# Kernel optimization log

Hardware: AMD Instinct MI355X
Metric: run time of the kernel (lower is better)

Reference implementation:

```python
import jax, jax.numpy as jnp
import numpy as np
import math

NLAT, NLON, LMAX, MMAX = 128, 256, 50, 50
M = NLAT * NLON  # = 2*NLAT^2 grid points, matches torch meshgrid(arange(nlat), arange(-nlat,nlat))

def _grid_np():
    gx, gy = np.meshgrid(np.arange(NLAT), np.arange(-NLAT, NLAT), indexing='ij')
    g = np.stack([gx.ravel(), gy.ravel()], -1).astype(np.float32)
    return g / NLAT * np.pi  # (M, 2)

def _cc_weights(n):
    # Clenshaw-Curtis quadrature nodes theta_j = pi*j/(n-1) and weights on [-1,1]
    N = n - 1
    theta = np.pi * np.arange(n) / N
    k = np.arange(1, N // 2 + 1)
    b = np.where(2 * k == N, 1.0, 2.0)
    S = (b / (4.0 * k ** 2 - 1.0) * np.cos(2.0 * np.outer(theta, k))).sum(-1)
    w = (2.0 / N) * (1.0 - S)
    w[0] *= 0.5
    w[-1] *= 0.5
    return theta, w

def _legendre(lmax, mmax, theta):
    # orthonormal (4pi-normalized) associated Legendre P_l^m(cos theta), Condon-Shortley phase
    x, s = np.cos(theta), np.sin(theta)
    P = np.zeros((mmax, lmax, theta.shape[0]))
    P[0, 0] = math.sqrt(1.0 / (4.0 * math.pi))
    pmm = P[0, 0].copy()
    for m in range(1, mmax):
        pmm = -math.sqrt((2 * m + 1) / (2.0 * m)) * s * pmm
        P[m, m] = pmm
    for m in range(mmax):
        if m + 1 < lmax:
            P[m, m + 1] = math.sqrt(2 * m + 3.0) * x * P[m, m]
        for l in range(m + 2, lmax):
            a = math.sqrt((4.0 * l * l - 1.0) / (l * l - m * m))
            bb = math.sqrt(((l - 1.0) ** 2 - m * m) / (4.0 * (l - 1.0) ** 2 - 1.0))
            P[m, l] = a * (x * P[m, l - 1] - bb * P[m, l - 2])
    return P

_theta_q, _wq = _cc_weights(NLAT)
_SHT_W = jnp.asarray((_legendre(LMAX, MMAX, _theta_q) * _wq).astype(np.float32))  # (mmax, lmax, nlat)
_GRID = jnp.asarray(_grid_np())  # (M, 2)

def setup_inputs() -> dict:
    key = jax.random.key(0)
    target = jax.random.normal(key, (2, 2048, 3), dtype=jnp.float32)
    return {"target": target}

def reference(target):
    B, N, _ = target.shape
    # to_spherical: rho=(B,N) features, sph=(phi, theta)-pi shift on theta -> (B,N,2)
    rho = jnp.linalg.norm(target, axis=-1)
    phi = jnp.arctan2(target[..., 1], target[..., 0])
    theta = jnp.arccos(target[..., 2] / rho)
    sph = jnp.stack([phi, theta - jnp.pi], axis=-1)  # (B, N, 2)
    # squared distances grid(M,2) vs sph(B,N,2) -> (B,M,N) via gram trick (no (B,M,N,2) temp)
    s2 = jnp.sum(sph * sph, -1)                 # (B, N)
    g2 = jnp.sum(_GRID * _GRID, -1)             # (M,)
    cross = jnp.einsum('md,bnd->bmn', _GRID, sph)
    D2 = jax.lax.stop_gradient(s2[:, None, :] + g2[None, :, None] - 2.0 * cross)
    _, idx = jax.lax.top_k(-D2, 3)              # (B, M, 3), 3-NN targets per grid point, ascending dist
    bidx = jnp.arange(B)[:, None, None]
    tmp = sph[bidx, idx]                        # (B, M, 3, 2)
    dist = jnp.sqrt(jnp.sum((tmp - _GRID[None, :, None, :]) ** 2, -1))  # (B, M, 3)
    w = dist / jnp.sum(dist, -1, keepdims=True)
    # three_interpolate: weighted combine of rho at 3 NNs -> (B, M)
    interp = jnp.sum(rho[bidx, idx] * w, -1)
    f = interp.reshape(B, NLAT, NLON)
    # RealSHT (equiangular grid): forward-normalized rfft over lon, then Legendre contraction over lat
    F = (2.0 * jnp.pi) * jnp.fft.rfft(f, axis=-1) / NLON  # (B, nlat, nlon//2+1) complex
    coeff_re = jnp.einsum('bkm,mlk->blm', jnp.real(F[..., :MMAX]), _SHT_W)  # (B, lmax, mmax)
    return coeff_re
```

## Files before the change

kernel.cpp:

```cpp
#include <hip/hip_runtime.h>
#include <math.h>
#include <stdint.h>

#define NLAT 128
#define NLON 256
#define LMAX 50
#define MMAX 50
#define MGRID (NLAT*NLON)
#define BATCH 2
#define NPTS 2048
#define NBKT 64
#define NSRT 2056
#define PI_F 3.14159265358979323846f

typedef float v2f __attribute__((ext_vector_type(2)));

__device__ __forceinline__ uint32_t umin32(uint32_t a, uint32_t b) { return a < b ? a : b; }
__device__ __forceinline__ uint32_t umax32(uint32_t a, uint32_t b) { return a > b ? a : b; }

#define WS_F    0
#define WS_SXY  65536
#define WS_SR   (WS_SXY + BATCH*NSRT*2)
#define WS_BST  (WS_SR + BATCH*NSRT)
#define WS_WG   78080
#define WS_CT   (WS_WG + MMAX*LMAX*NLAT)

__global__ __launch_bounds__(512)
void k_prep(const float* __restrict__ target, float* __restrict__ ws) {
    __shared__ __attribute__((aligned(16))) float2 s_all[NSRT];
    __shared__ float    s_rall[NSRT];
    __shared__ int      cnt[NBKT], start[NBKT + 1], cur[NBKT];
    __shared__ float    s_a[LMAX], s_bb[LMAX], s_w[NLAT];
    __shared__ float    s_cm;
    int blk = blockIdx.x;
    int tid = threadIdx.x;

    if (blk < BATCH) {
        const float* tg = target + blk * NPTS * 3;
        if (tid < NBKT) cnt[tid] = 0;
        __syncthreads();
        float ph[4], py[4], rh[4]; int bk[4];
        #pragma unroll
        for (int c = 0; c < 4; ++c) {
            int p = tid + c * 512;
            float x = tg[p*3], y = tg[p*3+1], z = tg[p*3+2];
            float r = sqrtf(fmaf(x, x, fmaf(y, y, z*z)));
            float cc = fminf(1.f, fmaxf(-1.f, z / r));
            float pyv = acosf(cc) - PI_F;
            ph[c] = atan2f(y, x); py[c] = pyv; rh[c] = r;
            int bb = (int)floorf((pyv + PI_F) * ((float)NBKT / PI_F));
            bk[c] = min(NBKT-1, max(0, bb));
            atomicAdd(&cnt[bk[c]], 1);
        }
        __syncthreads();
        if (tid < 64) {
            int v = cnt[tid];
            int cv = v;
            #pragma unroll
            for (int sh = 1; sh < 64; sh <<= 1) {
                int t = __shfl_up(v, sh);
                if (tid >= sh) v += t;
            }
            start[tid + 1] = v;
            cur[tid] = v - cv;
            if (tid == 0) start[0] = 0;
        }
        __syncthreads();
        #pragma unroll
        for (int c = 0; c < 4; ++c) {
            int pos = atomicAdd(&cur[bk[c]], 1);
            s_all[pos]  = make_float2(ph[c], py[c]);
            s_rall[pos] = rh[c];
        }
        if (tid < 8) {
            s_all[NPTS + tid] = make_float2(1e15f, 1e15f);
            s_rall[NPTS + tid] = 0.f;
        }
        __syncthreads();
        float2* gxy = (float2*)(ws + WS_SXY) + blk * NSRT;
        float*  gr  = ws + WS_SR + blk * NSRT;
        int*    bst = (int*)(ws + WS_BST) + blk * (NBKT + 1);
        for (int t = tid; t < NSRT; t += 512) { gxy[t] = s_all[t]; gr[t] = s_rall[t]; }
        if (tid <= NBKT) bst[tid] = start[tid];
    } else {
        int m = blk - BATCH;
        if (tid < 64) {
            int i = tid;
            float v = (i >= 1 && i <= m)
                      ? 0.5f * __log2f((2.f*i + 1.f) / (2.f*i)) : 0.f;
            #pragma unroll
            for (int sh = 1; sh < 64; sh <<= 1) v += __shfl_xor(v, sh);
            if (i == 0) s_cm = ((m & 1) ? -1.f : 1.f) * exp2f(v);
        } else if (tid < 128) {
            int l = tid - 64;
            if (l < LMAX) {
                float fl = (float)l, fm2 = (float)(m*m);
                s_a[l]  = sqrtf((4.f*fl*fl - 1.f) / fmaxf(fl*fl - fm2, 0.25f));
                float flm1 = fl - 1.f;
                s_bb[l] = sqrtf(fmaxf(flm1*flm1 - fm2, 0.f) /
                                fmaxf(4.f*flm1*flm1 - 1.f, 0.25f));
            }
        } else if (tid < 256) {
            int k = tid - 128;
            float theta = (PI_F * (float)k) / 127.0f;
            float S = 0.0f;
            for (int kk = 1; kk <= 63; ++kk)
                S += 2.0f / (4.0f*kk*kk - 1.0f) * __cosf(2.0f * theta * (float)kk);
            float w = (2.0f/127.0f) * (1.0f - S);
            if (k == 0 || k == NLAT-1) w *= 0.5f;
            s_w[k] = w;
        } else {
            int j = tid - 256;
            ws[WS_CT + m*256 + j] =
                __cosf((float)((m * j) & 255) * (2.0f*PI_F/256.0f));
        }
        __syncthreads();
        if (tid < NLAT) {
            int k = tid;
            float* Wm = ws + WS_WG + m * (LMAX * NLAT);
            float theta = (PI_F * (float)k) / 127.0f;
            float x = __cosf(theta), sn = __sinf(theta);
            float w = s_w[k];
            float pmm;
            if (m == 0) pmm = 0.28209479177f;
            else {
                float mag = exp2f((float)m * __log2f(fabsf(sn)));
                float sg  = (sn < 0.f && (m & 1)) ? -1.f : 1.f;
                pmm = 0.28209479177f * s_cm * mag * sg;
            }
            for (int l = 0; l < m; ++l) Wm[l*NLAT + k] = 0.0f;
            float Plm2 = pmm;
            Wm[m*NLAT + k] = Plm2 * w;
            if (m + 1 < LMAX) {
                float Plm1 = sqrtf(2.0f*m + 3.0f) * x * pmm;
                Wm[(m+1)*NLAT + k] = Plm1 * w;
                for (int l = m + 2; l < LMAX; ++l) {
                    float P = s_a[l] * fmaf(-s_bb[l], Plm2, x * Plm1);
                    Wm[l*NLAT + k] = P * w;
                    Plm2 = Plm1; Plm1 = P;
                }
            }
        }
    }
}

__global__ __launch_bounds__(512, 2)
void k_nn(const float* __restrict__ ws_c, float* __restrict__ f) {
    __shared__ __attribute__((aligned(16))) float2 s_all[NSRT];
    __shared__ float    s_rall[NSRT];
    __shared__ uint32_t s_keys[8*64*3];
    __shared__ int      s_start[NBKT + 1];
    __shared__ int      s_win[2];
    int b = blockIdx.x >> 8;
    int j = blockIdx.x & 255;
    int tid = threadIdx.x;

    if (tid <= NBKT)
        s_start[tid] = ((const int*)(ws_c + WS_BST))[b*(NBKT+1) + tid];
    __syncthreads();

    float gy = (float)(j - 128) * (PI_F / 128.0f);
    int c0 = (int)floorf((gy + PI_F) * ((float)NBKT / PI_F));
    c0 = min(NBKT-1, max(0, c0));
    if (tid < 64) {
        int t = tid;
        int lo_t = max(0, c0 - 5 - t), hi_t = min(NBKT-1, c0 + 5 + t);
        int cw_t = s_start[hi_t+1] - s_start[lo_t];
        unsigned long long ok =
            __ballot(cw_t >= 192 || (lo_t == 0 && hi_t == NBKT-1));
        int t0 = __ffsll((unsigned long long)ok) - 1;
        if (tid == 0) {
            s_win[0] = max(0, c0 - 5 - t0);
            s_win[1] = min(NBKT-1, c0 + 5 + t0);
        }
    }
    __syncthreads();

    int lo = s_win[0], hi = s_win[1];
    int off0 = s_start[lo];
    int cw   = s_start[hi+1] - off0;
    int n    = cw + 8;
    const float2* gxy = (const float2*)(ws_c + WS_SXY) + b * NSRT + off0;
    const float*  gr  = ws_c + WS_SR + b * NSRT + off0;
    for (int t = tid; t < n; t += 512) { s_all[t] = gxy[t]; s_rall[t] = gr[t]; }
    __syncthreads();

    int q = ((cw + 3) / 4 + 1) & ~1;
    int lane = tid & 63;
    int wv   = tid >> 6;
    int part = wv & 3;
    int lat  = lane + ((wv >> 2) << 6);
    float gx = (float)lat * (PI_F / 128.0f);
    v2f gx2 = {gx, gx}, gy2 = {gy, gy};
    uint32_t k0 = ~0u, k1 = ~0u, k2 = ~0u;
    uint32_t nb = (uint32_t)(part * q);
    const float4* p4 = (const float4*)(s_all + part * q);
    int iters = q >> 1;
    #pragma unroll 4
    for (int i = 0; i < iters; ++i) {
        float4 Q = p4[i];
        v2f px = {Q.x, Q.z}, pyy = {Q.y, Q.w};
        v2f dp = gx2 - px, dt = gy2 - pyy;
        v2f d = dp * dp;
        d = dt * dt + d;
        uint32_t key0 = (__float_as_uint(d.x) & 0xFFFFF800u) | (nb + 2u*i);
        uint32_t key1 = (__float_as_uint(d.y) & 0xFFFFF800u) | (nb + 2u*i + 1u);
        uint32_t t1;
        t1 = umin32(umax32(key0, k0), k1);
        k2 = umin32(umax32(key0, k1), k2);
        k0 = umin32(key0, k0); k1 = t1;
        t1 = umin32(umax32(key1, k0), k1);
        k2 = umin32(umax32(key1, k1), k2);
        k0 = umin32(key1, k0); k1 = t1;
    }
    s_keys[(wv*64 + lane)*3 + 0] = k0;
    s_keys[(wv*64 + lane)*3 + 1] = k1;
    s_keys[(wv*64 + lane)*3 + 2] = k2;
    __syncthreads();

    if (tid < 128) {
        int lane2 = tid & 63;
        int half  = tid >> 6;
        uint32_t m0 = ~0u, m1 = ~0u, m2 = ~0u;
        #pragma unroll
        for (int w = half*4; w < half*4 + 4; ++w) {
            #pragma unroll
            for (int s = 0; s < 3; ++s) {
                uint32_t key = s_keys[(w*64 + lane2)*3 + s];
                uint32_t t1 = umin32(umax32(key, m0), m1);
                m2 = umin32(umax32(key, m1), m2);
                m0 = umin32(key, m0); m1 = t1;
            }
        }
        int i0 = (int)(m0 & 2047);
        int i1 = (int)(m1 & 2047);
        int i2 = (int)(m2 & 2047);
        int lat2 = lane2 + (half << 6);
        float gxs = (float)lat2 * (PI_F / 128.0f);
        float2 p0 = s_all[i0], p1 = s_all[i1], p2 = s_all[i2];
        float e, r0, r1, r2;
        e = gxs - p0.x; r0 = e*e; e = gy - p0.y; r0 = sqrtf(fmaf(e, e, r0));
        e = gxs - p1.x; r1 = e*e; e = gy - p1.y; r1 = sqrtf(fmaf(e, e, r1));
        e = gxs - p2.x; r2 = e*e; e = gy - p2.y; r2 = sqrtf(fmaf(e, e, r2));
        float sum = r0 + r1 + r2;
        float interp = (s_rall[i0]*r0 + s_rall[i1]*r1 + s_rall[i2]*r2) / sum;
        f[b * MGRID + lat2 * NLON + j] = interp;
    }
}

__global__ __launch_bounds__(512)
void k_fft(const float* __restrict__ f, const float* __restrict__ ws_c,
           float* __restrict__ out) {
    __shared__ float red[NLAT*5];
    __shared__ float sFre[NLAT];
    __shared__ float cred[256];
    __shared__ float ct_s[256];
    int b = blockIdx.x / MMAX;
    int m = blockIdx.x % MMAX;
    int tid = threadIdx.x;

    if (tid < 256) ct_s[tid] = ws_c[WS_CT + m*256 + tid];
    __syncthreads();

    {
        int k = tid >> 2, g = tid & 3;
        const float4* fb4 = (const float4*)(f + b * MGRID);
        float p = 0.0f;
        int j0 = g * 64;
        #pragma unroll
        for (int i = 0; i < 16; ++i) {
            float4 v = fb4[k * 64 + g * 16 + i];
            p = fmaf(v.x, ct_s[j0 + 4*i    ], p);
            p = fmaf(v.y, ct_s[j0 + 4*i + 1], p);
            p = fmaf(v.z, ct_s[j0 + 4*i + 2], p);
            p = fmaf(v.w, ct_s[j0 + 4*i + 3], p);
        }
        red[k * 5 + g] = p;
    }
    __syncthreads();

    if (tid < NLAT) {
        int k = tid;
        sFre[k] = (red[k*5] + red[k*5+1] + red[k*5+2] + red[k*5+3])
                  * (2.0f * PI_F / 256.0f);
    }
    __syncthreads();

    float acc = 0.0f;
    if (tid < 200) {
        int l = tid >> 2, kq = tid & 3;
        const float* Wm = ws_c + WS_WG + (m * LMAX + l) * NLAT;
        #pragma unroll 8
        for (int i = 0; i < 32; ++i)
            acc = fmaf(Wm[kq*32 + i], sFre[kq*32 + i], acc);
    }
    if (tid < 256) cred[tid] = acc;
    __syncthreads();
    if (tid < LMAX)
        out[(b*LMAX + tid)*MMAX + m] =
            cred[4*tid] + cred[4*tid+1] + cred[4*tid+2] + cred[4*tid+3];
}

extern "C" void kernel_launch(void* const* d_in, const int* in_sizes, int n_in,
                              void* d_out, int out_size, void* d_ws, size_t ws_size,
                              hipStream_t stream) {
    const float* target = (const float*)d_in[0];
    float* out = (float*)d_out;
    float* ws  = (float*)d_ws;
    float* f   = ws + WS_F;

    k_prep<<<BATCH + MMAX, 512, 0, stream>>>(target, ws);
    k_nn  <<<BATCH * NLON, 512, 0, stream>>>(ws, f);
    k_fft <<<BATCH * MMAX, 512, 0, stream>>>(f, ws, out);
}
```

Before: 77.39 us.

## Fuse prep, NN interpolation and SHT into one cooperative kernel with grid syncs

Merges the three kernels into a single cooperative launch of 256 blocks, separating the phases with grid-wide syncs instead of kernel boundaries. Each block now handles two longitude columns in the NN phase, where before it handled one across 512 blocks. This removes two launch gaps and the tail effects between them. In exchange it halves the block count in the NN phase, adds grid-sync overhead, and raises register and LDS pressure because one kernel now declares every phase's shared arrays.

```diff
diff --git a/kernel.cpp b/kernel.cpp
--- a/kernel.cpp
+++ b/kernel.cpp
@@ -1,6 +1,9 @@
 #include <hip/hip_runtime.h>
+#include <hip/hip_cooperative_groups.h>
 #include <math.h>
 #include <stdint.h>
+
+namespace cg = cooperative_groups;
 
 #define NLAT 128
 #define NLON 256
@@ -25,13 +28,21 @@
 #define WS_WG   78080
 #define WS_CT   (WS_WG + MMAX*LMAX*NLAT)
 
-__global__ __launch_bounds__(512)
-void k_prep(const float* __restrict__ target, float* __restrict__ ws) {
+__global__ __launch_bounds__(512, 2)
+void k_fused(const float* __restrict__ target, float* ws, float* out) {
     __shared__ __attribute__((aligned(16))) float2 s_all[NSRT];
     __shared__ float    s_rall[NSRT];
-    __shared__ int      cnt[NBKT], start[NBKT + 1], cur[NBKT];
+    __shared__ uint32_t s_keys[8*64*3];
+    __shared__ int      cnt[NBKT], s_start[NBKT + 1], cur[NBKT];
+    __shared__ int      s_win[2];
     __shared__ float    s_a[LMAX], s_bb[LMAX], s_w[NLAT];
     __shared__ float    s_cm;
+    __shared__ float    red[NLAT*5];
+    __shared__ float    sFre[NLAT];
+    __shared__ float    cred[256];
+    __shared__ float    ct_s[256];
+
+    cg::grid_group grid = cg::this_grid();
     int blk = blockIdx.x;
     int tid = threadIdx.x;
 
@@ -61,9 +72,9 @@
                 int t = __shfl_up(v, sh);
                 if (tid >= sh) v += t;
             }
-            start[tid + 1] = v;
+            s_start[tid + 1] = v;
             cur[tid] = v - cv;
-            if (tid == 0) start[0] = 0;
+            if (tid == 0) s_start[0] = 0;
         }
         __syncthreads();
         #pragma unroll
@@ -81,8 +92,8 @@
         float*  gr  = ws + WS_SR + blk * NSRT;
         int*    bst = (int*)(ws + WS_BST) + blk * (NBKT + 1);
         for (int t = tid; t < NSRT; t += 512) { gxy[t] = s_all[t]; gr[t] = s_rall[t]; }
-        if (tid <= NBKT) bst[tid] = start[tid];
-    } else {
+        if (tid <= NBKT) bst[tid] = s_start[tid];
+    } else if (blk < BATCH + MMAX) {
         int m = blk - BATCH;
         if (tid < 64) {
             int i = tid;
@@ -142,163 +153,157 @@
             }
         }
     }
-}
-
-__global__ __launch_bounds__(512, 2)
-void k_nn(const float* __restrict__ ws_c, float* __restrict__ f) {
-    __shared__ __attribute__((aligned(16))) float2 s_all[NSRT];
-    __shared__ float    s_rall[NSRT];
-    __shared__ uint32_t s_keys[8*64*3];
-    __shared__ int      s_start[NBKT + 1];
-    __shared__ int      s_win[2];
-    int b = blockIdx.x >> 8;
-    int j = blockIdx.x & 255;
-    int tid = threadIdx.x;
-
-    if (tid <= NBKT)
-        s_start[tid] = ((const int*)(ws_c + WS_BST))[b*(NBKT+1) + tid];
-    __syncthreads();
-
-    float gy = (float)(j - 128) * (PI_F / 128.0f);
-    int c0 = (int)floorf((gy + PI_F) * ((float)NBKT / PI_F));
-    c0 = min(NBKT-1, max(0, c0));
-    if (tid < 64) {
-        int t = tid;
-        int lo_t = max(0, c0 - 5 - t), hi_t = min(NBKT-1, c0 + 5 + t);
-        int cw_t = s_start[hi_t+1] - s_start[lo_t];
-        unsigned long long ok =
-            __ballot(cw_t >= 192 || (lo_t == 0 && hi_t == NBKT-1));
-        int t0 = __ffsll((unsigned long long)ok) - 1;
-        if (tid == 0) {
-            s_win[0] = max(0, c0 - 5 - t0);
-            s_win[1] = min(NBKT-1, c0 + 5 + t0);
+    __threadfence();
+    grid.sync();
+
+    {
+        int b  = blk >> 7;
+        int jj = blk & 127;
+        if (tid <= NBKT)
+            s_start[tid] = ((const int*)(ws + WS_BST))[b*(NBKT+1) + tid];
+        __syncthreads();
+
+        for (int cidx = 0; cidx < 2; ++cidx) {
+            int j = jj * 2 + cidx;
+            float gy = (float)(j - 128) * (PI_F / 128.0f);
+            int c0 = (int)floorf((gy + PI_F) * ((float)NBKT / PI_F));
+            c0 = min(NBKT-1, max(0, c0));
+            if (tid < 64) {
+                int t = tid;
+                int lo_t = max(0, c0 - 5 - t), hi_t = min(NBKT-1, c0 + 5 + t);
+                int cw_t = s_start[hi_t+1] - s_start[lo_t];
+                unsigned long long ok =
+                    __ballot(cw_t >= 192 || (lo_t == 0 && hi_t == NBKT-1));
+                int t0 = __ffsll((unsigned long long)ok) - 1;
+                if (tid == 0) {
+                    s_win[0] = max(0, c0 - 5 - t0);
+                    s_win[1] = min(NBKT-1, c0 + 5 + t0);
+                }
+            }
+            __syncthreads();
+
+            int lo = s_win[0], hi = s_win[1];
+            int off0 = s_start[lo];
+            int cw   = s_start[hi+1] - off0;
+            int n    = cw + 8;
+            const float2* gxy = (const float2*)(ws + WS_SXY) + b * NSRT + off0;
+            const float*  gr  = ws + WS_SR + b * NSRT + off0;
+            for (int t = tid; t < n; t += 512) { s_all[t] = gxy[t]; s_rall[t] = gr[t]; }
+            __syncthreads();
+
+            int q = ((cw + 3) / 4 + 1) & ~1;
+            int lane = tid & 63;
+            int wv   = tid >> 6;
+            int part = wv & 3;
+            int lat  = lane + ((wv >> 2) << 6);
+            float gx = (float)lat * (PI_F / 128.0f);
+            v2f gx2 = {gx, gx}, gy2 = {gy, gy};
+            uint32_t k0 = ~0u, k1 = ~0u, k2 = ~0u;
+            uint32_t nb = (uint32_t)(part * q);
+            const float4* p4 = (const float4*)(s_all + part * q);
+            int iters = q >> 1;
+            #pragma unroll 4
+            for (int i = 0; i < iters; ++i) {
+                float4 Q = p4[i];
+                v2f px = {Q.x, Q.z}, pyy = {Q.y, Q.w};
+                v2f dp = gx2 - px, dt = gy2 - pyy;
+                v2f d = dp * dp;
+                d = dt * dt + d;
+                uint32_t key0 = (__float_as_uint(d.x) & 0xFFFFF800u) | (nb + 2u*i);
+                uint32_t key1 = (__float_as_uint(d.y) & 0xFFFFF800u) | (nb + 2u*i + 1u);
+                uint32_t t1;
+                t1 = umin32(umax32(key0, k0), k1);
+                k2 = umin32(umax32(key0, k1), k2);
+                k0 = umin32(key0, k0); k1 = t1;
+                t1 = umin32(umax32(key1, k0), k1);
+                k2 = umin32(umax32(key1, k1), k2);
+                k0 = umin32(key1, k0); k1 = t1;
+            }
+            s_keys[(wv*64 + lane)*3 + 0] = k0;
+            s_keys[(wv*64 + lane)*3 + 1] = k1;
+            s_keys[(wv*64 + lane)*3 + 2] = k2;
+            __syncthreads();
+
+            if (tid < 128) {
+                int lane2 = tid & 63;
+                int half  = tid >> 6;
+                uint32_t m0 = ~0u, m1 = ~0u, m2 = ~0u;
+                #pragma unroll
+                for (int w = half*4; w < half*4 + 4; ++w) {
+                    #pragma unroll
+                    for (int s = 0; s < 3; ++s) {
+                        uint32_t key = s_keys[(w*64 + lane2)*3 + s];
+                        uint32_t t1 = umin32(umax32(key, m0), m1);
+                        m2 = umin32(umax32(key, m1), m2);
+                        m0 = umin32(key, m0); m1 = t1;
+                    }
+                }
+                int i0 = (int)(m0 & 2047);
+                int i1 = (int)(m1 & 2047);
+                int i2 = (int)(m2 & 2047);
+                int lat2 = lane2 + (half << 6);
+                float gxs = (float)lat2 * (PI_F / 128.0f);
+                float2 p0 = s_all[i0], p1 = s_all[i1], p2 = s_all[i2];
+                float e, r0, r1, r2;
+                e = gxs - p0.x; r0 = e*e; e = gy - p0.y; r0 = sqrtf(fmaf(e, e, r0));
+                e = gxs - p1.x; r1 = e*e; e = gy - p1.y; r1 = sqrtf(fmaf(e, e, r1));
+                e = gxs - p2.x; r2 = e*e; e = gy - p2.y; r2 = sqrtf(fmaf(e, e, r2));
+                float sum = r0 + r1 + r2;
+                float interp = (s_rall[i0]*r0 + s_rall[i1]*r1 + s_rall[i2]*r2) / sum;
+                ws[WS_F + b * MGRID + lat2 * NLON + j] = interp;
+            }
+            __syncthreads();
         }
     }
-    __syncthreads();
-
-    int lo = s_win[0], hi = s_win[1];
-    int off0 = s_start[lo];
-    int cw   = s_start[hi+1] - off0;
-    int n    = cw + 8;
-    const float2* gxy = (const float2*)(ws_c + WS_SXY) + b * NSRT + off0;
-    const float*  gr  = ws_c + WS_SR + b * NSRT + off0;
-    for (int t = tid; t < n; t += 512) { s_all[t] = gxy[t]; s_rall[t] = gr[t]; }
-    __syncthreads();
-
-    int q = ((cw + 3) / 4 + 1) & ~1;
-    int lane = tid & 63;
-    int wv   = tid >> 6;
-    int part = wv & 3;
-    int lat  = lane + ((wv >> 2) << 6);
-    float gx = (float)lat * (PI_F / 128.0f);
-    v2f gx2 = {gx, gx}, gy2 = {gy, gy};
-    uint32_t k0 = ~0u, k1 = ~0u, k2 = ~0u;
-    uint32_t nb = (uint32_t)(part * q);
-    const float4* p4 = (const float4*)(s_all + part * q);
-    int iters = q >> 1;
-    #pragma unroll 4
-    for (int i = 0; i < iters; ++i) {
-        float4 Q = p4[i];
-        v2f px = {Q.x, Q.z}, pyy = {Q.y, Q.w};
-        v2f dp = gx2 - px, dt = gy2 - pyy;
-        v2f d = dp * dp;
-        d = dt * dt + d;
-        uint32_t key0 = (__float_as_uint(d.x) & 0xFFFFF800u) | (nb + 2u*i);
-        uint32_t key1 = (__float_as_uint(d.y) & 0xFFFFF800u) | (nb + 2u*i + 1u);
-        uint32_t t1;
-        t1 = umin32(umax32(key0, k0), k1);
-        k2 = umin32(umax32(key0, k1), k2);
-        k0 = umin32(key0, k0); k1 = t1;
-        t1 = umin32(umax32(key1, k0), k1);
-        k2 = umin32(umax32(key1, k1), k2);
-        k0 = umin32(key1, k0); k1 = t1;
+    __threadfence();
+    grid.sync();
+
+    if (blk >= BATCH * MMAX) return;
+    {
+        int b = blk / MMAX;
+        int m = blk % MMAX;
+
+        if (tid < 256) ct_s[tid] = ws[WS_CT + m*256 + tid];
+        __syncthreads();
+
+        {
+            int k = tid >> 2, g = tid & 3;
+            const float4* fb4 = (const float4*)(ws + WS_F + b * MGRID);
+            float p = 0.0f;
+            int j0 = g * 64;
+            #pragma unroll
+            for (int i = 0; i < 16; ++i) {
+                float4 v = fb4[k * 64 + g * 16 + i];
+                p = fmaf(v.x, ct_s[j0 + 4*i    ], p);
+                p = fmaf(v.y, ct_s[j0 + 4*i + 1], p);
+                p = fmaf(v.z, ct_s[j0 + 4*i + 2], p);
+                p = fmaf(v.w, ct_s[j0 + 4*i + 3], p);
+            }
+            red[k * 5 + g] = p;
+        }
+        __syncthreads();
+
+        if (tid < NLAT) {
+            int k = tid;
+            sFre[k] = (red[k*5] + red[k*5+1] + red[k*5+2] + red[k*5+3])
+                      * (2.0f * PI_F / 256.0f);
+        }
+        __syncthreads();
+
+        float acc = 0.0f;
+        if (tid < 200) {
+            int l = tid >> 2, kq = tid & 3;
+            const float* Wm = ws + WS_WG + (m * LMAX + l) * NLAT;
+            #pragma unroll 8
+            for (int i = 0; i < 32; ++i)
+                acc = fmaf(Wm[kq*32 + i], sFre[kq*32 + i], acc);
+        }
+        if (tid < 256) cred[tid] = acc;
+        __syncthreads();
+        if (tid < LMAX)
+            out[(b*LMAX + tid)*MMAX + m] =
+                cred[4*tid] + cred[4*tid+1] + cred[4*tid+2] + cred[4*tid+3];
     }
-    s_keys[(wv*64 + lane)*3 + 0] = k0;
-    s_keys[(wv*64 + lane)*3 + 1] = k1;
-    s_keys[(wv*64 + lane)*3 + 2] = k2;
-    __syncthreads();
-
-    if (tid < 128) {
-        int lane2 = tid & 63;
-        int half  = tid >> 6;
-        uint32_t m0 = ~0u, m1 = ~0u, m2 = ~0u;
-        #pragma unroll
-        for (int w = half*4; w < half*4 + 4; ++w) {
-            #pragma unroll
-            for (int s = 0; s < 3; ++s) {
-                uint32_t key = s_keys[(w*64 + lane2)*3 + s];
-                uint32_t t1 = umin32(umax32(key, m0), m1);
-                m2 = umin32(umax32(key, m1), m2);
-                m0 = umin32(key, m0); m1 = t1;
-            }
-        }
-        int i0 = (int)(m0 & 2047);
-        int i1 = (int)(m1 & 2047);
-        int i2 = (int)(m2 & 2047);
-        int lat2 = lane2 + (half << 6);
-        float gxs = (float)lat2 * (PI_F / 128.0f);
-        float2 p0 = s_all[i0], p1 = s_all[i1], p2 = s_all[i2];
-        float e, r0, r1, r2;
-        e = gxs - p0.x; r0 = e*e; e = gy - p0.y; r0 = sqrtf(fmaf(e, e, r0));
-        e = gxs - p1.x; r1 = e*e; e = gy - p1.y; r1 = sqrtf(fmaf(e, e, r1));
-        e = gxs - p2.x; r2 = e*e; e = gy - p2.y; r2 = sqrtf(fmaf(e, e, r2));
-        float sum = r0 + r1 + r2;
-        float interp = (s_rall[i0]*r0 + s_rall[i1]*r1 + s_rall[i2]*r2) / sum;
-        f[b * MGRID + lat2 * NLON + j] = interp;
-    }
-}
-
-__global__ __launch_bounds__(512)
-void k_fft(const float* __restrict__ f, const float* __restrict__ ws_c,
-           float* __restrict__ out) {
-    __shared__ float red[NLAT*5];
-    __shared__ float sFre[NLAT];
-    __shared__ float cred[256];
-    __shared__ float ct_s[256];
-    int b = blockIdx.x / MMAX;
-    int m = blockIdx.x % MMAX;
-    int tid = threadIdx.x;
-
-    if (tid < 256) ct_s[tid] = ws_c[WS_CT + m*256 + tid];
-    __syncthreads();
-
-    {
-        int k = tid >> 2, g = tid & 3;
-        const float4* fb4 = (const float4*)(f + b * MGRID);
-        float p = 0.0f;
-        int j0 = g * 64;
-        #pragma unroll
-        for (int i = 0; i < 16; ++i) {
-            float4 v = fb4[k * 64 + g * 16 + i];
-            p = fmaf(v.x, ct_s[j0 + 4*i    ], p);
-            p = fmaf(v.y, ct_s[j0 + 4*i + 1], p);
-            p = fmaf(v.z, ct_s[j0 + 4*i + 2], p);
-            p = fmaf(v.w, ct_s[j0 + 4*i + 3], p);
-        }
-        red[k * 5 + g] = p;
-    }
-    __syncthreads();
-
-    if (tid < NLAT) {
-        int k = tid;
-        sFre[k] = (red[k*5] + red[k*5+1] + red[k*5+2] + red[k*5+3])
-                  * (2.0f * PI_F / 256.0f);
-    }
-    __syncthreads();
-
-    float acc = 0.0f;
-    if (tid < 200) {
-        int l = tid >> 2, kq = tid & 3;
-        const float* Wm = ws_c + WS_WG + (m * LMAX + l) * NLAT;
-        #pragma unroll 8
-        for (int i = 0; i < 32; ++i)
-            acc = fmaf(Wm[kq*32 + i], sFre[kq*32 + i], acc);
-    }
-    if (tid < 256) cred[tid] = acc;
-    __syncthreads();
-    if (tid < LMAX)
-        out[(b*LMAX + tid)*MMAX + m] =
-            cred[4*tid] + cred[4*tid+1] + cred[4*tid+2] + cred[4*tid+3];
 }
 
 extern "C" void kernel_launch(void* const* d_in, const int* in_sizes, int n_in,
@@ -307,9 +312,8 @@
     const float* target = (const float*)d_in[0];
     float* out = (float*)d_out;
     float* ws  = (float*)d_ws;
-    float* f   = ws + WS_F;
-
-    k_prep<<<BATCH + MMAX, 512, 0, stream>>>(target, ws);
-    k_nn  <<<BATCH * NLON, 512, 0, stream>>>(ws, f);
-    k_fft <<<BATCH * MMAX, 512, 0, stream>>>(f, ws, out);
+
+    void* args[] = { (void*)&target, (void*)&ws, (void*)&out };
+    hipLaunchCooperativeKernel((void*)k_fused, dim3(256), dim3(512),
+                               args, 0, stream);
 }
```

Result: slower. 224.0 us (+189.5%).
